# Kernel tuning notes

Hardware: AMD Instinct MI355X
Metric: run time of the kernel (lower is better)

Reference implementation:

```python
import jax, jax.numpy as jnp
import numpy as np

N_NODES = 50000
DEG = 32
WIDTH = 128
DEPTH = 2
BATCH = 4096
EPS = 1e-12  # F.normalize default eps


def setup_inputs() -> dict:
    key = jax.random.key(0)
    k1, k2, k3, k4, k5, k6, k7 = jax.random.split(key, 7)
    nbd = jax.random.randint(k1, (N_NODES, DEG), 0, N_NODES, dtype=jnp.int32)
    node_idx = jax.random.randint(k2, (BATCH,), 0, N_NODES, dtype=jnp.int32)
    feats = jax.random.normal(k3, (BATCH, WIDTH), dtype=jnp.float32)
    s = 1.0 / np.sqrt(WIDTH)
    W_agg = jax.random.normal(k4, (WIDTH, WIDTH), dtype=jnp.float32) * s
    b_agg = jax.random.normal(k5, (WIDTH,), dtype=jnp.float32) * s
    W_lin = jax.random.normal(k6, (WIDTH, 2 * WIDTH), dtype=jnp.float32) * s
    b_lin = jax.random.normal(k7, (WIDTH,), dtype=jnp.float32) * s
    return {"nbd": nbd, "node_idx": node_idx, "feats": feats,
            "W_agg": W_agg, "b_agg": b_agg, "W_lin": W_lin, "b_lin": b_lin}


def reference(nbd, node_idx, feats, W_agg, b_agg, W_lin, b_lin):
    # H0: zero features for every graph node except the batch nodes (dict-of-zeros + row assignment in original)
    H = jnp.zeros((N_NODES, WIDTH), dtype=feats.dtype).at[node_idx].set(feats)
    for _ in range(DEPTH):  # combine Linear is weight-shared across hops (ModuleList([layer]*depth))
        # aggregator MLP applied once per node, then gathered per neighbor
        M = jax.nn.relu(H @ W_agg.T + b_agg)            # [N, d]
        agg = jnp.max(M[nbd], axis=1)                    # [N, deg, d] -> [N, d] max-pool aggregate
        h = jax.nn.relu(jnp.concatenate([H, agg], axis=-1) @ W_lin.T + b_lin)  # [N, d]
        norm = jnp.sqrt(jnp.sum(h * h, axis=-1, keepdims=True))
        H = h / jnp.maximum(norm, EPS)                   # F.normalize(dim=0) on 1d vector == per-row l2 norm
    return H[node_idx]                                   # [batch, width]
```

## Files before the change

### kernel.cpp

```cpp
#include <hip/hip_runtime.h>
#include <math.h>

#define N_NODES 50000
#define DEG 32
#define WIDTH 128
#define BATCH 4096
#define EPS 1e-12f

typedef __attribute__((ext_vector_type(8))) short short8;
typedef __attribute__((ext_vector_type(4))) float f32x4;
typedef unsigned short u16;

__device__ __forceinline__ u16 f2bf(float f) {
    unsigned x;
    __builtin_memcpy(&x, &f, 4);
    unsigned r = (x + 0x7fff + ((x >> 16) & 1)) >> 16;
    return (u16)r;
}
__device__ __forceinline__ unsigned pkmax_u16(unsigned a, unsigned b) {
    unsigned lo = (a & 0xffffu) > (b & 0xffffu) ? (a & 0xffffu) : (b & 0xffffu);
    unsigned hi = (a >> 16) > (b >> 16) ? (a >> 16) : (b >> 16);
    return lo | (hi << 16);
}
__device__ __forceinline__ short8 cvt8(const float* __restrict__ p) {
    float4 a0 = *(const float4*)p;
    float4 a1 = *(const float4*)(p + 4);
    short8 v;
    v[0] = (short)f2bf(a0.x); v[1] = (short)f2bf(a0.y);
    v[2] = (short)f2bf(a0.z); v[3] = (short)f2bf(a0.w);
    v[4] = (short)f2bf(a1.x); v[5] = (short)f2bf(a1.y);
    v[6] = (short)f2bf(a1.z); v[7] = (short)f2bf(a1.w);
    return v;
}

__global__ __launch_bounds__(512) void head_k(
    const float* __restrict__ feats, const float* __restrict__ W_agg,
    const float* __restrict__ W_lin, const float* __restrict__ b_agg,
    const int* __restrict__ node_idx, int* __restrict__ inv,
    u16* __restrict__ M0b, float* __restrict__ S) {
    __shared__ u16 wa[128 * 128];
    __shared__ u16 wl[128 * 128];

    int tid = threadIdx.x;
    int gid = blockIdx.x * 512 + tid;
    if (gid < BATCH) atomicMax(&inv[node_idx[gid]], gid);

#pragma unroll
    for (int it = 0; it < 4; ++it) {
        int c = tid + it * 512;
        int r = c >> 4, ch = c & 15;
        int sw = (ch * 16) ^ ((r & 7) << 4);
        *(short8*)((char*)wa + r * 256 + sw) = cvt8(W_agg + (size_t)r * 128 + ch * 8);
        *(short8*)((char*)wl + r * 256 + sw) = cvt8(W_lin + (size_t)r * 256 + ch * 8);
    }

    int w = tid >> 6, l = tid & 63, li = l & 15, kq = l >> 4;
    int r0 = blockIdx.x * 16;
    int arow = r0 + li;
    int col = w * 16 + li;

    short8 a[4];
#pragma unroll
    for (int kk = 0; kk < 4; ++kk)
        a[kk] = cvt8(feats + (size_t)arow * 128 + kk * 32 + kq * 8);
    __syncthreads();

    f32x4 am = (f32x4){0,0,0,0}, as = (f32x4){0,0,0,0};
#pragma unroll
    for (int kk = 0; kk < 4; ++kk) {
        int sw = (kk * 64 + kq * 16) ^ ((col & 7) << 4);
        short8 bm = *(const short8*)((char*)wa + col * 256 + sw);
        am = __builtin_amdgcn_mfma_f32_16x16x32_bf16(a[kk], bm, am, 0, 0, 0);
        short8 bs = *(const short8*)((char*)wl + col * 256 + sw);
        as = __builtin_amdgcn_mfma_f32_16x16x32_bf16(a[kk], bs, as, 0, 0, 0);
    }

    float ba = b_agg[col];
#pragma unroll
    for (int r = 0; r < 4; ++r) {
        int grow = r0 + kq * 4 + r;
        float t = am[r] + ba;
        t = t > 0.f ? t : 0.f;
        M0b[(size_t)grow * 128 + col] = f2bf(t);
        S[(size_t)grow * 128 + col] = as[r];
    }
}

__global__ __launch_bounds__(256) void agg1_k(
    const int* __restrict__ nbd, const int* __restrict__ inv,
    const u16* __restrict__ M0b, const float* __restrict__ b_agg,
    unsigned* __restrict__ AGG1u) {
    int wave = blockIdx.x * 4 + (threadIdx.x >> 6);
    int lane = threadIdx.x & 63;
    int n0 = wave * 2;

    int nb = nbd[(size_t)n0 * DEG + lane];
    int bi = inv[nb];
    unsigned long long warm = __ballot(bi >= 0);
    unsigned m0 = (unsigned)warm;
    unsigned m1 = (unsigned)(warm >> 32);

    float ba0 = b_agg[2 * lane], ba1 = b_agg[2 * lane + 1];
    ba0 = ba0 > 0.f ? ba0 : 0.f;
    ba1 = ba1 > 0.f ? ba1 : 0.f;
    unsigned rb = (unsigned)f2bf(ba0) | ((unsigned)f2bf(ba1) << 16);

    unsigned acc0 = (m0 != 0xffffffffu) ? rb : 0u;
    while (m0) {
        int pos = __builtin_ctz(m0);
        m0 &= m0 - 1;
        int bib = __shfl(bi, pos);
        acc0 = pkmax_u16(acc0, ((const unsigned*)(M0b + (size_t)bib * WIDTH))[lane]);
    }
    AGG1u[(size_t)n0 * 64 + lane] = acc0;

    unsigned acc1 = (m1 != 0xffffffffu) ? rb : 0u;
    while (m1) {
        int pos = __builtin_ctz(m1);
        m1 &= m1 - 1;
        int bib = __shfl(bi, 32 + pos);
        acc1 = pkmax_u16(acc1, ((const unsigned*)(M0b + (size_t)bib * WIDTH))[lane]);
    }
    AGG1u[(size_t)(n0 + 1) * 64 + lane] = acc1;
}

__global__ __launch_bounds__(512) void hop1a_k(
    const u16* __restrict__ AGG1, const int* __restrict__ inv,
    const float* __restrict__ S, const float* __restrict__ b_lin,
    const float* __restrict__ W_lin, u16* __restrict__ H1g) {
    __shared__ u16 wlds[128 * 128];
    __shared__ float pnorm[2 * 64];

    int tid = threadIdx.x;
    int w = tid >> 6, l = tid & 63, li = l & 15, kq = l >> 4;
    int rg = w >> 1, cg = w & 1;
    int row0 = blockIdx.x * 64;
    int lrow = rg * 16 + li;
    int arow = row0 + lrow;
    if (arow > N_NODES - 1) arow = N_NODES - 1;

    short8 af[4];
#pragma unroll
    for (int kk = 0; kk < 4; ++kk)
        af[kk] = *(const short8*)(AGG1 + (size_t)arow * 128 + kk * 32 + kq * 8);

#pragma unroll
    for (int it = 0; it < 4; ++it) {
        int c = tid + it * 512;
        int r = c >> 4, ch = c & 15;
        *(short8*)((char*)wlds + r * 256 + ((ch * 16) ^ ((r & 7) << 4))) =
            cvt8(W_lin + (size_t)r * 256 + 128 + ch * 8);
    }
    __syncthreads();

    f32x4 h[4];
#pragma unroll
    for (int n = 0; n < 4; ++n) h[n] = (f32x4){0,0,0,0};
#pragma unroll
    for (int kk = 0; kk < 4; ++kk)
#pragma unroll
        for (int n = 0; n < 4; ++n) {
            int col = cg * 64 + n * 16 + li;
            short8 b = *(const short8*)((char*)wlds + col * 256 +
                                        ((kk * 64 + kq * 16) ^ ((col & 7) << 4)));
            h[n] = __builtin_amdgcn_mfma_f32_16x16x32_bf16(af[kk], b, h[n], 0, 0, 0);
        }

    float blv[4];
#pragma unroll
    for (int n = 0; n < 4; ++n) blv[n] = b_lin[cg * 64 + n * 16 + li];

    float v[4][4];
#pragma unroll
    for (int r = 0; r < 4; ++r) {
        int lr = rg * 16 + kq * 4 + r;
        int grow = row0 + lr;
        int growc = grow < N_NODES ? grow : N_NODES - 1;
        int bi = inv[growc];
#pragma unroll
        for (int n = 0; n < 4; ++n) v[r][n] = h[n][r] + blv[n];
        if (bi >= 0) {
#pragma unroll
            for (int n = 0; n < 4; ++n)
                v[r][n] += S[(size_t)bi * 128 + cg * 64 + n * 16 + li];
        }
        float p = 0.f;
#pragma unroll
        for (int n = 0; n < 4; ++n) {
            v[r][n] = fmaxf(v[r][n], 0.f);
            p += v[r][n] * v[r][n];
        }
        p += __shfl_xor(p, 1);
        p += __shfl_xor(p, 2);
        p += __shfl_xor(p, 4);
        p += __shfl_xor(p, 8);
        if (li == 0) pnorm[cg * 64 + lr] = p;
    }
    __syncthreads();

#pragma unroll
    for (int r = 0; r < 4; ++r) {
        int lr = rg * 16 + kq * 4 + r;
        int grow = row0 + lr;
        float p = pnorm[lr] + pnorm[64 + lr];
        float sc = 1.0f / fmaxf(sqrtf(p), EPS);
        if (grow < N_NODES) {
#pragma unroll
            for (int n = 0; n < 4; ++n)
                H1g[(size_t)grow * 128 + cg * 64 + n * 16 + li] = f2bf(v[r][n] * sc);
        }
    }
}

__global__ __launch_bounds__(512) void m1_k(
    const u16* __restrict__ H1g, const float* __restrict__ b_agg,
    const float* __restrict__ W_agg, u16* __restrict__ M1) {
    __shared__ u16 wlds[128 * 128];

    int tid = threadIdx.x;
    int w = tid >> 6, l = tid & 63, li = l & 15, kq = l >> 4;
    int rg = w >> 1, cg = w & 1;
    int row0 = blockIdx.x * 64;
    int arow = row0 + rg * 16 + li;
    if (arow > N_NODES - 1) arow = N_NODES - 1;

    short8 af[4];
#pragma unroll
    for (int kk = 0; kk < 4; ++kk)
        af[kk] = *(const short8*)(H1g + (size_t)arow * 128 + kk * 32 + kq * 8);

#pragma unroll
    for (int it = 0; it < 4; ++it) {
        int c = tid + it * 512;
        int r = c >> 4, ch = c & 15;
        *(short8*)((char*)wlds + r * 256 + ((ch * 16) ^ ((r & 7) << 4))) =
            cvt8(W_agg + (size_t)r * 128 + ch * 8);
    }
    __syncthreads();

    f32x4 m[4];
#pragma unroll
    for (int n = 0; n < 4; ++n) m[n] = (f32x4){0,0,0,0};
#pragma unroll
    for (int kk = 0; kk < 4; ++kk)
#pragma unroll
        for (int n = 0; n < 4; ++n) {
            int col = cg * 64 + n * 16 + li;
            short8 b = *(const short8*)((char*)wlds + col * 256 +
                                        ((kk * 64 + kq * 16) ^ ((col & 7) << 4)));
            m[n] = __builtin_amdgcn_mfma_f32_16x16x32_bf16(af[kk], b, m[n], 0, 0, 0);
        }

    float bav[4];
#pragma unroll
    for (int n = 0; n < 4; ++n) bav[n] = b_agg[cg * 64 + n * 16 + li];
#pragma unroll
    for (int r = 0; r < 4; ++r) {
        int grow = row0 + rg * 16 + kq * 4 + r;
        if (grow < N_NODES) {
#pragma unroll
            for (int n = 0; n < 4; ++n) {
                float t = m[n][r] + bav[n];
                t = t > 0.f ? t : 0.f;
                M1[(size_t)grow * 128 + cg * 64 + n * 16 + li] = f2bf(t);
            }
        }
    }
}

__global__ __launch_bounds__(512) void tail_k(
    const int* __restrict__ nbd, const int* __restrict__ node_idx,
    const u16* __restrict__ H1g, const u16* __restrict__ M1,
    const float* __restrict__ W_lin, const float* __restrict__ b_lin,
    float* __restrict__ out) {
    __shared__ u16 wt[128 * 256];
    __shared__ u16 ab2[16 * 264];
    __shared__ float pn[128];
    __shared__ float pnt[16];

    int tid = threadIdx.x;
    int w = tid >> 6, l = tid & 63, li = l & 15, kq = l >> 4;
    int row0 = blockIdx.x * 16;

#pragma unroll
    for (int it = 0; it < 8; ++it) {
        int c = tid + it * 512;
        int r = c >> 5, ch = c & 31;
        *(short8*)((char*)wt + r * 512 + ((ch * 16) ^ ((r & 7) << 4))) =
            cvt8(W_lin + (size_t)r * 256 + ch * 8);
    }

#pragma unroll
    for (int rr = 0; rr < 2; ++rr) {
        int lr = w * 2 + rr;
        int i = row0 + lr;
        int n = node_idx[i];
        unsigned hv = ((const unsigned*)(H1g + (size_t)n * 128))[l];
        *(unsigned*)((char*)ab2 + lr * 528 + l * 4) = hv;
        int nb = (l < DEG) ? nbd[(size_t)n * DEG + l] : 0;
        unsigned acc = 0;
#pragma unroll
        for (int j = 0; j < DEG; ++j) {
            int bib = __shfl(nb, j);
            acc = pkmax_u16(acc, ((const unsigned*)(M1 + (size_t)bib * 128))[l]);
        }
        *(unsigned*)((char*)ab2 + lr * 528 + 256 + l * 4) = acc;
    }
    __syncthreads();

    int col = w * 16 + li;
    f32x4 acc4 = (f32x4){0,0,0,0};
#pragma unroll
    for (int kk = 0; kk < 8; ++kk) {
        short8 a = *(const short8*)((char*)ab2 + li * 528 + kk * 64 + kq * 16);
        short8 b = *(const short8*)((char*)wt + col * 512 +
                                    ((kk * 64 + kq * 16) ^ ((col & 7) << 4)));
        acc4 = __builtin_amdgcn_mfma_f32_16x16x32_bf16(a, b, acc4, 0, 0, 0);
    }

    float bl = b_lin[col];
    float v[4];
#pragma unroll
    for (int r = 0; r < 4; ++r) {
        v[r] = fmaxf(acc4[r] + bl, 0.f);
        float p = v[r] * v[r];
        p += __shfl_xor(p, 1);
        p += __shfl_xor(p, 2);
        p += __shfl_xor(p, 4);
        p += __shfl_xor(p, 8);
        if (li == 0) pn[w * 16 + kq * 4 + r] = p;
    }
    __syncthreads();
    if (tid < 16) {
        float s = 0.f;
#pragma unroll
        for (int ww = 0; ww < 8; ++ww) s += pn[ww * 16 + tid];
        pnt[tid] = s;
    }
    __syncthreads();
#pragma unroll
    for (int r = 0; r < 4; ++r) {
        int row = kq * 4 + r;
        float sc = 1.0f / fmaxf(sqrtf(pnt[row]), EPS);
        out[(size_t)(row0 + row) * 128 + col] = v[r] * sc;
    }
}

extern "C" void kernel_launch(void* const* d_in, const int* in_sizes, int n_in,
                              void* d_out, int out_size, void* d_ws, size_t ws_size,
                              hipStream_t stream) {
    const int*   nbd      = (const int*)d_in[0];
    const int*   node_idx = (const int*)d_in[1];
    const float* feats    = (const float*)d_in[2];
    const float* W_agg    = (const float*)d_in[3];
    const float* b_agg    = (const float*)d_in[4];
    const float* W_lin    = (const float*)d_in[5];
    const float* b_lin    = (const float*)d_in[6];
    float* out = (float*)d_out;

    char* base = (char*)d_ws;
    size_t off = 0;
    int* inv  = (int*)(base + off);   off += 50048 * 4;
    u16* M0b  = (u16*)(base + off);   off += (size_t)BATCH * 128 * 2;
    float* S  = (float*)(base + off); off += (size_t)BATCH * 128 * 4;
    u16* AGG1 = (u16*)(base + off);   off += (size_t)N_NODES * 128 * 2;
    u16* H1g  = (u16*)(base + off);   off += (size_t)N_NODES * 128 * 2;
    u16* M1   = (u16*)(base + off);   off += (size_t)N_NODES * 128 * 2;

    hipMemsetAsync(inv, 0xFF, 50048 * 4, stream);

    head_k<<<BATCH / 16, 512, 0, stream>>>(feats, W_agg, W_lin, b_agg, node_idx, inv, M0b, S);

    agg1_k<<<N_NODES / 8, 256, 0, stream>>>(nbd, inv, M0b, b_agg, (unsigned*)AGG1);

    hop1a_k<<<(N_NODES + 63) / 64, 512, 0, stream>>>(AGG1, inv, S, b_lin, W_lin, H1g);

    m1_k<<<(N_NODES + 63) / 64, 512, 0, stream>>>(H1g, b_agg, W_agg, M1);

    tail_k<<<BATCH / 16, 512, 0, stream>>>(nbd, node_idx, H1g, M1, W_lin, b_lin, out);
}
```

Baseline: 63.47 us.

## Fuse hop-1 combine with M1 matmul and precompute bf16 weights once

Merges the hop-1 combine kernel and the M1 aggregator matmul into one kernel. The normalized H1 tile stays in LDS and feeds the second MFMA directly, which removes one launch and the full H1 read-back for M1. H1 is now written to global only for batch nodes, since only tail_k reads those rows. The head kernel's block 0 converts W_lin and W_agg to bf16 once into workspace, so later kernels skip per-block fp32 loads and conversion. This adds LDS use and a launch-bounds occupancy hint, and the later kernels depend on head_k having written the converted weights.

New measurement: 61.03 us. -3.8%, faster.

```diff
diff --git a/kernel.cpp b/kernel.cpp
--- a/kernel.cpp
+++ b/kernel.cpp
@@ -37,7 +37,8 @@
     const float* __restrict__ feats, const float* __restrict__ W_agg,
     const float* __restrict__ W_lin, const float* __restrict__ b_agg,
     const int* __restrict__ node_idx, int* __restrict__ inv,
-    u16* __restrict__ M0b, float* __restrict__ S) {
+    u16* __restrict__ M0b, float* __restrict__ S,
+    u16* __restrict__ Wab_ws, u16* __restrict__ Wlb_ws) {
     __shared__ u16 wa[128 * 128];
     __shared__ u16 wl[128 * 128];
 
@@ -83,6 +84,19 @@
         t = t > 0.f ? t : 0.f;
         M0b[(size_t)grow * 128 + col] = f2bf(t);
         S[(size_t)grow * 128 + col] = as[r];
+    }
+
+    if (blockIdx.x == 0) {
+#pragma unroll
+        for (int it = 0; it < 8; ++it) {
+            int i = tid + it * 512;
+            *(short8*)(Wlb_ws + (size_t)i * 8) = cvt8(W_lin + (size_t)i * 8);
+        }
+#pragma unroll
+        for (int it = 0; it < 4; ++it) {
+            int i = tid + it * 512;
+            *(short8*)(Wab_ws + (size_t)i * 8) = cvt8(W_agg + (size_t)i * 8);
+        }
     }
 }
 
@@ -124,11 +138,14 @@
     AGG1u[(size_t)(n0 + 1) * 64 + lane] = acc1;
 }
 
-__global__ __launch_bounds__(512) void hop1a_k(
+__global__ __launch_bounds__(512, 6) void hop1mm_k(
     const u16* __restrict__ AGG1, const int* __restrict__ inv,
     const float* __restrict__ S, const float* __restrict__ b_lin,
-    const float* __restrict__ W_lin, u16* __restrict__ H1g) {
+    const float* __restrict__ b_agg,
+    const u16* __restrict__ Wlb, const u16* __restrict__ Wab,
+    u16* __restrict__ H1g, u16* __restrict__ M1) {
     __shared__ u16 wlds[128 * 128];
+    __shared__ u16 h1t[64 * 136];
     __shared__ float pnorm[2 * 64];
 
     int tid = threadIdx.x;
@@ -149,7 +166,7 @@
         int c = tid + it * 512;
         int r = c >> 4, ch = c & 15;
         *(short8*)((char*)wlds + r * 256 + ((ch * 16) ^ ((r & 7) << 4))) =
-            cvt8(W_lin + (size_t)r * 256 + 128 + ch * 8);
+            *(const short8*)(Wlb + (size_t)r * 256 + 128 + ch * 8);
     }
     __syncthreads();
 
@@ -171,18 +188,19 @@
     for (int n = 0; n < 4; ++n) blv[n] = b_lin[cg * 64 + n * 16 + li];
 
     float v[4][4];
+    int biA[4];
 #pragma unroll
     for (int r = 0; r < 4; ++r) {
         int lr = rg * 16 + kq * 4 + r;
         int grow = row0 + lr;
         int growc = grow < N_NODES ? grow : N_NODES - 1;
-        int bi = inv[growc];
+        biA[r] = inv[growc];
 #pragma unroll
         for (int n = 0; n < 4; ++n) v[r][n] = h[n][r] + blv[n];
-        if (bi >= 0) {
+        if (biA[r] >= 0) {
 #pragma unroll
             for (int n = 0; n < 4; ++n)
-                v[r][n] += S[(size_t)bi * 128 + cg * 64 + n * 16 + li];
+                v[r][n] += S[(size_t)biA[r] * 128 + cg * 64 + n * 16 + li];
         }
         float p = 0.f;
 #pragma unroll
@@ -204,39 +222,32 @@
         int grow = row0 + lr;
         float p = pnorm[lr] + pnorm[64 + lr];
         float sc = 1.0f / fmaxf(sqrtf(p), EPS);
-        if (grow < N_NODES) {
+        u16 vb[4];
+#pragma unroll
+        for (int n = 0; n < 4; ++n) vb[n] = f2bf(v[r][n] * sc);
+        if (grow < N_NODES && biA[r] >= 0) {
 #pragma unroll
             for (int n = 0; n < 4; ++n)
-                H1g[(size_t)grow * 128 + cg * 64 + n * 16 + li] = f2bf(v[r][n] * sc);
-        }
-    }
-}
-
-__global__ __launch_bounds__(512) void m1_k(
-    const u16* __restrict__ H1g, const float* __restrict__ b_agg,
-    const float* __restrict__ W_agg, u16* __restrict__ M1) {
-    __shared__ u16 wlds[128 * 128];
-
-    int tid = threadIdx.x;
-    int w = tid >> 6, l = tid & 63, li = l & 15, kq = l >> 4;
-    int rg = w >> 1, cg = w & 1;
-    int row0 = blockIdx.x * 64;
-    int arow = row0 + rg * 16 + li;
-    if (arow > N_NODES - 1) arow = N_NODES - 1;
-
-    short8 af[4];
-#pragma unroll
-    for (int kk = 0; kk < 4; ++kk)
-        af[kk] = *(const short8*)(H1g + (size_t)arow * 128 + kk * 32 + kq * 8);
+                H1g[(size_t)grow * 128 + cg * 64 + n * 16 + li] = vb[n];
+        }
+#pragma unroll
+        for (int n = 0; n < 4; ++n) h1t[lr * 136 + cg * 64 + n * 16 + li] = vb[n];
+    }
+    __syncthreads();
 
 #pragma unroll
     for (int it = 0; it < 4; ++it) {
         int c = tid + it * 512;
         int r = c >> 4, ch = c & 15;
         *(short8*)((char*)wlds + r * 256 + ((ch * 16) ^ ((r & 7) << 4))) =
-            cvt8(W_agg + (size_t)r * 128 + ch * 8);
-    }
-    __syncthreads();
+            *(const short8*)(Wab + (size_t)r * 128 + ch * 8);
+    }
+    __syncthreads();
+
+    short8 af2[4];
+#pragma unroll
+    for (int kk = 0; kk < 4; ++kk)
+        af2[kk] = *(const short8*)(h1t + lrow * 136 + kk * 32 + kq * 8);
 
     f32x4 m[4];
 #pragma unroll
@@ -248,7 +259,7 @@
             int col = cg * 64 + n * 16 + li;
             short8 b = *(const short8*)((char*)wlds + col * 256 +
                                         ((kk * 64 + kq * 16) ^ ((col & 7) << 4)));
-            m[n] = __builtin_amdgcn_mfma_f32_16x16x32_bf16(af[kk], b, m[n], 0, 0, 0);
+            m[n] = __builtin_amdgcn_mfma_f32_16x16x32_bf16(af2[kk], b, m[n], 0, 0, 0);
         }
 
     float bav[4];
@@ -271,7 +282,7 @@
 __global__ __launch_bounds__(512) void tail_k(
     const int* __restrict__ nbd, const int* __restrict__ node_idx,
     const u16* __restrict__ H1g, const u16* __restrict__ M1,
-    const float* __restrict__ W_lin, const float* __restrict__ b_lin,
+    const u16* __restrict__ Wlb, const float* __restrict__ b_lin,
     float* __restrict__ out) {
     __shared__ u16 wt[128 * 256];
     __shared__ u16 ab2[16 * 264];
@@ -287,7 +298,7 @@
         int c = tid + it * 512;
         int r = c >> 5, ch = c & 31;
         *(short8*)((char*)wt + r * 512 + ((ch * 16) ^ ((r & 7) << 4))) =
-            cvt8(W_lin + (size_t)r * 256 + ch * 8);
+            *(const short8*)(Wlb + (size_t)r * 256 + ch * 8);
     }
 
 #pragma unroll
@@ -361,6 +372,8 @@
     char* base = (char*)d_ws;
     size_t off = 0;
     int* inv  = (int*)(base + off);   off += 50048 * 4;
+    u16* Wab  = (u16*)(base + off);   off += 16384 * 2;
+    u16* Wlb  = (u16*)(base + off);   off += 32768 * 2;
     u16* M0b  = (u16*)(base + off);   off += (size_t)BATCH * 128 * 2;
     float* S  = (float*)(base + off); off += (size_t)BATCH * 128 * 4;
     u16* AGG1 = (u16*)(base + off);   off += (size_t)N_NODES * 128 * 2;
@@ -369,13 +382,13 @@
 
     hipMemsetAsync(inv, 0xFF, 50048 * 4, stream);
 
-    head_k<<<BATCH / 16, 512, 0, stream>>>(feats, W_agg, W_lin, b_agg, node_idx, inv, M0b, S);
+    head_k<<<BATCH / 16, 512, 0, stream>>>(feats, W_agg, W_lin, b_agg, node_idx, inv,
+                                           M0b, S, Wab, Wlb);
 
     agg1_k<<<N_NODES / 8, 256, 0, stream>>>(nbd, inv, M0b, b_agg, (unsigned*)AGG1);
 
-    hop1a_k<<<(N_NODES + 63) / 64, 512, 0, stream>>>(AGG1, inv, S, b_lin, W_lin, H1g);
-
-    m1_k<<<(N_NODES + 63) / 64, 512, 0, stream>>>(H1g, b_agg, W_agg, M1);
-
-    tail_k<<<BATCH / 16, 512, 0, stream>>>(nbd, node_idx, H1g, M1, W_lin, b_lin, out);
-}
+    hop1mm_k<<<(N_NODES + 63) / 64, 512, 0, stream>>>(
+        AGG1, inv, S, b_lin, b_agg, Wlb, Wab, H1g, M1);
+
+    tail_k<<<BATCH / 16, 512, 0, stream>>>(nbd, node_idx, H1g, M1, Wlb, b_lin, out);
+}
```
